# Optimization experiments

Hardware: AMD Instinct MI355X
Metric: run time of the kernel (lower is better)

Reference implementation:

```python
import jax, jax.numpy as jnp
import numpy as np

DIM = 1024
CTX_DIM = 1024
HEADS = 8
DIM_HEAD = 64
INNER = HEADS * DIM_HEAD  # 512
EPS = 1e-5


def _layer_norm(x, gamma, beta):
    mu = jnp.mean(x, axis=-1, keepdims=True)
    var = jnp.mean(jnp.square(x - mu), axis=-1, keepdims=True)
    return (x - mu) * jax.lax.rsqrt(var + EPS) * gamma + beta


def setup_inputs() -> dict:
    key = jax.random.key(0)
    ks = jax.random.split(key, 8)
    b, n, m = 4, 2048, 2048
    x = jax.random.normal(ks[0], (b, n, DIM), dtype=jnp.float32)
    context = jax.random.normal(ks[1], (b, m, CTX_DIM), dtype=jnp.float32)
    Wq = jax.random.normal(ks[2], (DIM, INNER), dtype=jnp.float32) / np.sqrt(DIM)
    Wkv = jax.random.normal(ks[3], (CTX_DIM, 2 * INNER), dtype=jnp.float32) / np.sqrt(CTX_DIM)
    Wout = jax.random.normal(ks[4], (INNER, DIM), dtype=jnp.float32) / np.sqrt(INNER)
    bout = jnp.zeros((DIM,), dtype=jnp.float32)
    g1 = jnp.ones((DIM,), dtype=jnp.float32)
    b1 = jnp.zeros((DIM,), dtype=jnp.float32)
    g2 = jnp.ones((CTX_DIM,), dtype=jnp.float32)
    b2 = jnp.zeros((CTX_DIM,), dtype=jnp.float32)
    return {"x": x, "context": context, "g1": g1, "b1": b1, "g2": g2, "b2": b2,
            "Wq": Wq, "Wkv": Wkv, "Wout": Wout, "bout": bout}


def reference(x, context, g1, b1, g2, b2, Wq, Wkv, Wout, bout):
    b, n, _ = x.shape
    m = context.shape[1]
    scale = DIM_HEAD ** -0.5
    xn = _layer_norm(x, g1, b1)
    cn = _layer_norm(context, g2, b2)
    q = xn @ Wq                      # [b, n, inner]
    kv = cn @ Wkv                    # [b, m, 2*inner]
    k, v = jnp.split(kv, 2, axis=-1)
    # split heads: [b, h, seq, d]
    q = q.reshape(b, n, HEADS, DIM_HEAD).transpose(0, 2, 1, 3)
    k = k.reshape(b, m, HEADS, DIM_HEAD).transpose(0, 2, 1, 3)
    v = v.reshape(b, m, HEADS, DIM_HEAD).transpose(0, 2, 1, 3)
    sim = jnp.einsum('bhid,bhjd->bhij', q, k) * scale
    attn = jax.nn.softmax(sim, axis=-1)
    out = jnp.einsum('bhij,bhjd->bhid', attn, v)
    out = out.transpose(0, 2, 1, 3).reshape(b, n, INNER)
    return out @ Wout + bout
```

## Files before the change

### kernel.cpp

```cpp
#include <hip/hip_runtime.h>
#include <hip/hip_bf16.h>

typedef __bf16 bf16_t;
typedef bf16_t bf16x4 __attribute__((ext_vector_type(4)));
typedef bf16_t bf16x8 __attribute__((ext_vector_type(8)));
typedef float floatx4 __attribute__((ext_vector_type(4)));

typedef __attribute__((address_space(1))) const unsigned char* gptr_t;
typedef __attribute__((address_space(3))) unsigned char* lptr_t;

#define BATCH 4
#define SEQ_N 2048
#define SEQ_M 2048
#define DIM 1024
#define INNER 512
#define HEADS 8
#define DHEAD 64
#define QSCALE 0.18033688011112042f

__device__ __forceinline__ void wtrans_tile(const float* W, bf16_t* Wt,
                                            int K, int N, int n0, int k0, float scale) {
    __shared__ bf16_t T[64][72];
    const int tid = threadIdx.x;
#pragma unroll
    for (int p = 0; p < 2; p++) {
        int r = (tid >> 3) + p * 32;
        int c = (tid & 7) * 8;
        const float* src = W + (size_t)(k0 + r) * N + n0 + c;
        float4 v0 = *(const float4*)src;
        float4 v1 = *(const float4*)(src + 4);
        T[r][c + 0] = (bf16_t)(v0.x * scale); T[r][c + 1] = (bf16_t)(v0.y * scale);
        T[r][c + 2] = (bf16_t)(v0.z * scale); T[r][c + 3] = (bf16_t)(v0.w * scale);
        T[r][c + 4] = (bf16_t)(v1.x * scale); T[r][c + 5] = (bf16_t)(v1.y * scale);
        T[r][c + 6] = (bf16_t)(v1.z * scale); T[r][c + 7] = (bf16_t)(v1.w * scale);
    }
    __syncthreads();
#pragma unroll
    for (int p = 0; p < 2; p++) {
        int rn = (tid >> 3) + p * 32;
        int ck = (tid & 7) * 8;
        bf16x8 v;
#pragma unroll
        for (int i = 0; i < 8; i++) v[i] = T[ck + i][rn];
        *(bf16x8*)(Wt + (size_t)(n0 + rn) * K + k0 + ck) = v;
    }
}

__device__ __forceinline__ void ln_row(const float* in, const float* g,
                                       const float* bt, bf16_t* out, int row) {
    const int tid = threadIdx.x;
    float4 xv = ((const float4*)(in + (size_t)row * 1024))[tid];
    float s = xv.x + xv.y + xv.z + xv.w;
    float ss = xv.x * xv.x + xv.y * xv.y + xv.z * xv.z + xv.w * xv.w;
#pragma unroll
    for (int off = 32; off > 0; off >>= 1) {
        s  += __shfl_down(s, off);
        ss += __shfl_down(ss, off);
    }
    __shared__ float red[8];
    const int wave = tid >> 6, lane = tid & 63;
    if (lane == 0) { red[wave] = s; red[4 + wave] = ss; }
    __syncthreads();
    if (tid == 0) {
        float a = red[0] + red[1] + red[2] + red[3];
        float b = red[4] + red[5] + red[6] + red[7];
        red[0] = a * (1.f / 1024.f);
        red[4] = b * (1.f / 1024.f);
    }
    __syncthreads();
    const float mu = red[0];
    const float var = red[4] - mu * mu;
    const float rs = rsqrtf(var + 1e-5f);

    float4 gv = ((const float4*)g)[tid];
    float4 bv = ((const float4*)bt)[tid];
    bf16x4 o;
    o[0] = (bf16_t)((xv.x - mu) * rs * gv.x + bv.x);
    o[1] = (bf16_t)((xv.y - mu) * rs * gv.y + bv.y);
    o[2] = (bf16_t)((xv.z - mu) * rs * gv.z + bv.z);
    o[3] = (bf16_t)((xv.w - mu) * rs * gv.w + bv.w);
    *(bf16x4*)(out + (size_t)row * 1024 + tid * 4) = o;
}

__global__ __launch_bounds__(256) void prep_kernel(const float* __restrict__ x,
                                                   const float* __restrict__ ctx,
                                                   const float* __restrict__ g1,
                                                   const float* __restrict__ b1,
                                                   const float* __restrict__ g2,
                                                   const float* __restrict__ b2,
                                                   const float* __restrict__ Wq,
                                                   const float* __restrict__ Wkv,
                                                   const float* __restrict__ Wout,
                                                   bf16_t* __restrict__ xn,
                                                   bf16_t* __restrict__ cn,
                                                   bf16_t* __restrict__ Wqt,
                                                   bf16_t* __restrict__ Wkvt,
                                                   bf16_t* __restrict__ Woutt) {
    int id = blockIdx.x;
    if (id < 128) {
        wtrans_tile(Wq, Wqt, 1024, 512, (id & 7) * 64, (id >> 3) * 64, QSCALE);
    } else if (id < 384) {
        int t = id - 128;
        wtrans_tile(Wkv, Wkvt, 1024, 1024, (t & 15) * 64, (t >> 4) * 64, 1.0f);
    } else if (id < 512) {
        int t = id - 384;
        wtrans_tile(Wout, Woutt, 512, 1024, (t & 15) * 64, (t >> 4) * 64, 1.0f);
    } else {
        int rid = id - 512;
        if (rid < BATCH * SEQ_N) ln_row(x, g1, b1, xn, rid);
        else                     ln_row(ctx, g2, b2, cn, rid - BATCH * SEQ_N);
    }
}

template <int MODE, typename OutT>
__device__ __forceinline__ void gemm_body(const bf16_t* __restrict__ A,
                                          const bf16_t* __restrict__ Bt,
                                          OutT* __restrict__ C,
                                          const float* __restrict__ bias,
                                          int ldC, int K, int row0, int col0) {
    __shared__ bf16_t As[128 * 64];
    __shared__ bf16_t Bs[128 * 64];
    const int tid = threadIdx.x;
    const int wave = tid >> 6, lane = tid & 63;
    const int wr = (wave >> 1) * 64, wc = (wave & 1) * 64;
    const int quad = lane >> 4, l16 = lane & 15;

    floatx4 acc[4][4] = {};

    for (int k0 = 0; k0 < K; k0 += 64) {
#pragma unroll
        for (int p = 0; p < 4; p++) {
            int cA = p * 256 + wave * 64 + lane;
            int rA = cA >> 3, kc = (cA & 7) * 8;
            __builtin_amdgcn_global_load_lds(
                (gptr_t)(A + (size_t)(row0 + rA) * K + k0 + kc),
                (lptr_t)(As + (size_t)(p * 256 + wave * 64) * 8), 16, 0, 0);
            __builtin_amdgcn_global_load_lds(
                (gptr_t)(Bt + (size_t)(col0 + rA) * K + k0 + kc),
                (lptr_t)(Bs + (size_t)(p * 256 + wave * 64) * 8), 16, 0, 0);
        }
        __syncthreads();
#pragma unroll
        for (int kt = 0; kt < 2; kt++) {
            bf16x8 aF[4], bF[4];
#pragma unroll
            for (int i = 0; i < 4; i++)
                aF[i] = *(bf16x8*)&As[(wr + i * 16 + l16) * 64 + kt * 32 + quad * 8];
#pragma unroll
            for (int j = 0; j < 4; j++)
                bF[j] = *(bf16x8*)&Bs[(wc + j * 16 + l16) * 64 + kt * 32 + quad * 8];
#pragma unroll
            for (int i = 0; i < 4; i++)
#pragma unroll
                for (int j = 0; j < 4; j++) {
                    if (MODE == 0)
                        acc[i][j] = __builtin_amdgcn_mfma_f32_16x16x32_bf16(
                            aF[i], bF[j], acc[i][j], 0, 0, 0);
                    else
                        acc[i][j] = __builtin_amdgcn_mfma_f32_16x16x32_bf16(
                            bF[j], aF[i], acc[i][j], 0, 0, 0);
                }
        }
        __syncthreads();
    }

    if (MODE == 0) {
#pragma unroll
        for (int i = 0; i < 4; i++)
#pragma unroll
            for (int j = 0; j < 4; j++) {
                int col = col0 + wc + j * 16 + l16;
                float bv = bias ? bias[col] : 0.f;
#pragma unroll
                for (int r = 0; r < 4; r++) {
                    int row = row0 + wr + i * 16 + quad * 4 + r;
                    C[(size_t)row * ldC + col] = (OutT)(acc[i][j][r] + bv);
                }
            }
    } else {
#pragma unroll
        for (int i = 0; i < 4; i++) {
            int grow = row0 + wr + i * 16 + l16;
            int bat = grow >> 11, m = grow & 2047;
#pragma unroll
            for (int j = 0; j < 4; j++)
#pragma unroll
                for (int r = 0; r < 4; r++) {
                    int d = col0 + wc + j * 16 + quad * 4 + r - 512;
                    C[((size_t)bat * 512 + d) * 2048 + m] = (OutT)acc[i][j][r];
                }
        }
    }
}

__global__ __launch_bounds__(256) void gemm_qkv_kernel(const bf16_t* __restrict__ xn,
                                                       const bf16_t* __restrict__ cn,
                                                       const bf16_t* __restrict__ Wqt,
                                                       const bf16_t* __restrict__ Wkvt,
                                                       bf16_t* __restrict__ qb,
                                                       bf16_t* __restrict__ kvb,
                                                       bf16_t* __restrict__ Vtg) {
    const int bx = blockIdx.x;
    const int row0 = blockIdx.y * 128;
    if (bx < 4)
        gemm_body<0, bf16_t>(xn, Wqt, qb, nullptr, 512, DIM, row0, bx * 128);
    else if (bx < 8)
        gemm_body<0, bf16_t>(cn, Wkvt, kvb, nullptr, 512, DIM, row0, (bx - 4) * 128);
    else
        gemm_body<1, bf16_t>(cn, Wkvt, Vtg, nullptr, 0, DIM, row0, (bx - 4) * 128);
}

__global__ __launch_bounds__(256) void gemm_out_kernel(const bf16_t* __restrict__ ao,
                                                       const bf16_t* __restrict__ Woutt,
                                                       float* __restrict__ out,
                                                       const float* __restrict__ bias) {
    gemm_body<0, float>(ao, Woutt, out, bias, DIM, INNER, blockIdx.y * 128, blockIdx.x * 128);
}

#define PSTR 72
__global__ __launch_bounds__(256) void attn_kernel(const bf16_t* __restrict__ q,
                                                   const bf16_t* __restrict__ kv,
                                                   const bf16_t* __restrict__ Vtg,
                                                   bf16_t* __restrict__ o) {
    __shared__ bf16_t Qs[64 * 72];
    __shared__ bf16_t Ks[64 * 72];
    __shared__ bf16_t Vs[80 * 72];

    const int b = blockIdx.z, h = blockIdx.y;
    const int n0 = blockIdx.x * 64;
    const int tid = threadIdx.x;
    const int wave = tid >> 6, lane = tid & 63;
    const int quad = lane >> 4, l16 = lane & 15;

    const int sr = (tid >> 3);
    const int sc = (tid & 7) * 8;

#pragma unroll
    for (int p = 0; p < 2; p++) {
        int r = sr + p * 32;
        *(bf16x8*)&Qs[r * 72 + sc] =
            *(const bf16x8*)(q + (size_t)(b * SEQ_N + n0 + r) * INNER + h * DHEAD + sc);
    }
#pragma unroll
    for (int i = 0; i < 4; i++) {
        int idx = i * 256 + tid;
        int r = 64 + (idx >> 6), c = idx & 63;
        Vs[r * 72 + c] = (r == 64) ? (bf16_t)1.0f : (bf16_t)0.0f;
    }

    bf16x8 kreg[2], vreg[2];
#pragma unroll
    for (int p = 0; p < 2; p++) {
        int r = sr + p * 32;
        kreg[p] = *(const bf16x8*)(kv + (size_t)(b * SEQ_M + r) * 512 + h * DHEAD + sc);
        vreg[p] = *(const bf16x8*)(Vtg + (size_t)((b * HEADS + h) * DHEAD + r) * SEQ_M + sc);
    }
    __syncthreads();

    bf16x8 aQ[2];
#pragma unroll
    for (int kt = 0; kt < 2; kt++)
        aQ[kt] = *(bf16x8*)&Qs[(wave * 16 + l16) * 72 + kt * 32 + quad * 8];

    bf16_t* Pw = Qs + wave * (16 * PSTR);

    floatx4 oacc[5] = {};

    for (int it = 0; it < SEQ_M / 64; ++it) {
        __syncthreads();
#pragma unroll
        for (int p = 0; p < 2; p++) {
            int r = sr + p * 32;
            *(bf16x8*)&Ks[r * 72 + sc] = kreg[p];
            *(bf16x8*)&Vs[r * 72 + sc] = vreg[p];
        }
        __syncthreads();

        if (it + 1 < SEQ_M / 64) {
            int m0 = (it + 1) * 64;
#pragma unroll
            for (int p = 0; p < 2; p++) {
                int r = sr + p * 32;
                kreg[p] = *(const bf16x8*)(kv + (size_t)(b * SEQ_M + m0 + r) * 512 + h * DHEAD + sc);
                vreg[p] = *(const bf16x8*)(Vtg + (size_t)((b * HEADS + h) * DHEAD + r) * SEQ_M + m0 + sc);
            }
        }

        floatx4 s[4] = {};
#pragma unroll
        for (int kt = 0; kt < 2; kt++)
#pragma unroll
            for (int jt = 0; jt < 4; jt++) {
                bf16x8 aK = *(bf16x8*)&Ks[(jt * 16 + l16) * 72 + kt * 32 + quad * 8];
                s[jt] = __builtin_amdgcn_mfma_f32_16x16x32_bf16(aK, aQ[kt], s[jt], 0, 0, 0);
            }

#pragma unroll
        for (int jt = 0; jt < 4; jt++) {
            bf16x4 pk;
#pragma unroll
            for (int r = 0; r < 4; r++) pk[r] = (bf16_t)exp2f(s[jt][r]);
            *(bf16x4*)&Pw[l16 * PSTR + jt * 16 + quad * 4] = pk;
        }

#pragma unroll
        for (int kt = 0; kt < 2; kt++) {
            bf16x8 aP = *(bf16x8*)&Pw[l16 * PSTR + kt * 32 + quad * 8];
#pragma unroll
            for (int dt = 0; dt < 5; dt++) {
                bf16x8 bV = *(bf16x8*)&Vs[(dt * 16 + l16) * 72 + kt * 32 + quad * 8];
                oacc[dt] = __builtin_amdgcn_mfma_f32_16x16x32_bf16(aP, bV, oacc[dt], 0, 0, 0);
            }
        }
    }

    float inv[4];
#pragma unroll
    for (int r = 0; r < 4; r++) {
        float l = __shfl(oacc[4][r], (int)(lane & 48));
        inv[r] = 1.0f / l;
    }
#pragma unroll
    for (int dt = 0; dt < 4; dt++)
#pragma unroll
        for (int r = 0; r < 4; r++) {
            int row = n0 + wave * 16 + quad * 4 + r;
            int col = h * DHEAD + dt * 16 + l16;
            o[(size_t)(b * SEQ_N + row) * INNER + col] =
                (bf16_t)(oacc[dt][r] * inv[r]);
        }
}

extern "C" void kernel_launch(void* const* d_in, const int* in_sizes, int n_in,
                              void* d_out, int out_size, void* d_ws, size_t ws_size,
                              hipStream_t stream) {
    const float* x    = (const float*)d_in[0];
    const float* ctx  = (const float*)d_in[1];
    const float* g1   = (const float*)d_in[2];
    const float* b1   = (const float*)d_in[3];
    const float* g2   = (const float*)d_in[4];
    const float* b2   = (const float*)d_in[5];
    const float* Wq   = (const float*)d_in[6];
    const float* Wkv  = (const float*)d_in[7];
    const float* Wout = (const float*)d_in[8];
    const float* bout = (const float*)d_in[9];
    float* out = (float*)d_out;

    const int rows = BATCH * SEQ_N;
    bf16_t* xn    = (bf16_t*)d_ws;
    bf16_t* cn    = xn + (size_t)rows * DIM;
    bf16_t* qb    = cn + (size_t)rows * DIM;
    bf16_t* kvb   = qb + (size_t)rows * INNER;
    bf16_t* Vtg   = kvb + (size_t)rows * INNER;
    bf16_t* Wqt   = Vtg + (size_t)rows * INNER;
    bf16_t* Wkvt  = Wqt + (size_t)INNER * DIM;
    bf16_t* Woutt = Wkvt + (size_t)(2 * INNER) * DIM;
    bf16_t* o_attn = xn;

    prep_kernel<<<512 + 2 * rows, 256, 0, stream>>>(
        x, ctx, g1, b1, g2, b2, Wq, Wkv, Wout, xn, cn, Wqt, Wkvt, Woutt);
    gemm_qkv_kernel<<<dim3(12, rows / 128), 256, 0, stream>>>(
        xn, cn, Wqt, Wkvt, qb, kvb, Vtg);
    attn_kernel<<<dim3(SEQ_N / 64, HEADS, BATCH), 256, 0, stream>>>(qb, kvb, Vtg, o_attn);
    gemm_out_kernel<<<dim3(DIM / 128, rows / 128), 256, 0, stream>>>(o_attn, Woutt, out, bout);
}
```

Measured before the change: 263.5 us.

## Rework layernorm, V-transpose epilogue, out-GEMM tiling and attention denominator

LayerNorm now has one wave handle a whole row, four rows per block. This drops the block-level shared-memory reduction and both barriers, and cuts the prep grid size. The transposed V store in the QKV GEMM is staged through LDS so it writes 4-wide vector stores instead of scattered scalar bf16 stores. The output GEMM gets a 64-column tile template, which doubles its block count. In attention, the all-ones row used to compute the softmax denominator moves from LDS into a register operand, and the K/V prefetch becomes unconditional. On the last iteration that prefetch reads just past the K/V and V-transposed buffers, into adjacent workspace.

```diff
diff --git a/kernel.cpp b/kernel.cpp
--- a/kernel.cpp
+++ b/kernel.cpp
@@ -46,40 +46,40 @@
     }
 }
 
-__device__ __forceinline__ void ln_row(const float* in, const float* g,
-                                       const float* bt, bf16_t* out, int row) {
-    const int tid = threadIdx.x;
-    float4 xv = ((const float4*)(in + (size_t)row * 1024))[tid];
-    float s = xv.x + xv.y + xv.z + xv.w;
-    float ss = xv.x * xv.x + xv.y * xv.y + xv.z * xv.z + xv.w * xv.w;
+__device__ __forceinline__ void ln_row_wave(const float* in, const float* g,
+                                            const float* bt, bf16_t* out, int row) {
+    const int lane = threadIdx.x & 63;
+    const float4* src = (const float4*)(in + (size_t)row * 1024);
+    float4 xv[4];
+    float s = 0.f, ss = 0.f;
+#pragma unroll
+    for (int k = 0; k < 4; k++) {
+        xv[k] = src[lane + k * 64];
+        s  += xv[k].x + xv[k].y + xv[k].z + xv[k].w;
+        ss += xv[k].x * xv[k].x + xv[k].y * xv[k].y + xv[k].z * xv[k].z + xv[k].w * xv[k].w;
+    }
 #pragma unroll
     for (int off = 32; off > 0; off >>= 1) {
         s  += __shfl_down(s, off);
         ss += __shfl_down(ss, off);
     }
-    __shared__ float red[8];
-    const int wave = tid >> 6, lane = tid & 63;
-    if (lane == 0) { red[wave] = s; red[4 + wave] = ss; }
-    __syncthreads();
-    if (tid == 0) {
-        float a = red[0] + red[1] + red[2] + red[3];
-        float b = red[4] + red[5] + red[6] + red[7];
-        red[0] = a * (1.f / 1024.f);
-        red[4] = b * (1.f / 1024.f);
-    }
-    __syncthreads();
-    const float mu = red[0];
-    const float var = red[4] - mu * mu;
+    s  = __shfl(s, 0);
+    ss = __shfl(ss, 0);
+    const float mu = s * (1.f / 1024.f);
+    const float var = ss * (1.f / 1024.f) - mu * mu;
     const float rs = rsqrtf(var + 1e-5f);
-
-    float4 gv = ((const float4*)g)[tid];
-    float4 bv = ((const float4*)bt)[tid];
-    bf16x4 o;
-    o[0] = (bf16_t)((xv.x - mu) * rs * gv.x + bv.x);
-    o[1] = (bf16_t)((xv.y - mu) * rs * gv.y + bv.y);
-    o[2] = (bf16_t)((xv.z - mu) * rs * gv.z + bv.z);
-    o[3] = (bf16_t)((xv.w - mu) * rs * gv.w + bv.w);
-    *(bf16x4*)(out + (size_t)row * 1024 + tid * 4) = o;
+    const float4* gp = (const float4*)g;
+    const float4* bp = (const float4*)bt;
+#pragma unroll
+    for (int k = 0; k < 4; k++) {
+        float4 gv = gp[lane + k * 64], bv = bp[lane + k * 64];
+        bf16x4 o;
+        o[0] = (bf16_t)((xv[k].x - mu) * rs * gv.x + bv.x);
+        o[1] = (bf16_t)((xv[k].y - mu) * rs * gv.y + bv.y);
+        o[2] = (bf16_t)((xv[k].z - mu) * rs * gv.z + bv.z);
+        o[3] = (bf16_t)((xv[k].w - mu) * rs * gv.w + bv.w);
+        *(bf16x4*)(out + (size_t)row * 1024 + (lane + k * 64) * 4) = o;
+    }
 }
 
 __global__ __launch_bounds__(256) void prep_kernel(const float* __restrict__ x,
@@ -106,26 +106,28 @@
         int t = id - 384;
         wtrans_tile(Wout, Woutt, 512, 1024, (t & 15) * 64, (t >> 4) * 64, 1.0f);
     } else {
-        int rid = id - 512;
-        if (rid < BATCH * SEQ_N) ln_row(x, g1, b1, xn, rid);
-        else                     ln_row(ctx, g2, b2, cn, rid - BATCH * SEQ_N);
-    }
-}
-
-template <int MODE, typename OutT>
+        int row = (id - 512) * 4 + (threadIdx.x >> 6);
+        if (row < BATCH * SEQ_N) ln_row_wave(x, g1, b1, xn, row);
+        else                     ln_row_wave(ctx, g2, b2, cn, row - BATCH * SEQ_N);
+    }
+}
+
+template <int NT, int MODE, typename OutT>
 __device__ __forceinline__ void gemm_body(const bf16_t* __restrict__ A,
                                           const bf16_t* __restrict__ Bt,
                                           OutT* __restrict__ C,
                                           const float* __restrict__ bias,
                                           int ldC, int K, int row0, int col0) {
     __shared__ bf16_t As[128 * 64];
-    __shared__ bf16_t Bs[128 * 64];
+    __shared__ bf16_t Bs[NT * 64];
     const int tid = threadIdx.x;
     const int wave = tid >> 6, lane = tid & 63;
-    const int wr = (wave >> 1) * 64, wc = (wave & 1) * 64;
+    constexpr int WC = NT / 2;
+    constexpr int NJ = WC / 16;
+    const int wr = (wave >> 1) * 64, wc = (wave & 1) * WC;
     const int quad = lane >> 4, l16 = lane & 15;
 
-    floatx4 acc[4][4] = {};
+    floatx4 acc[4][NJ] = {};
 
     for (int k0 = 0; k0 < K; k0 += 64) {
 #pragma unroll
@@ -135,24 +137,25 @@
             __builtin_amdgcn_global_load_lds(
                 (gptr_t)(A + (size_t)(row0 + rA) * K + k0 + kc),
                 (lptr_t)(As + (size_t)(p * 256 + wave * 64) * 8), 16, 0, 0);
-            __builtin_amdgcn_global_load_lds(
-                (gptr_t)(Bt + (size_t)(col0 + rA) * K + k0 + kc),
-                (lptr_t)(Bs + (size_t)(p * 256 + wave * 64) * 8), 16, 0, 0);
+            if (p < NT / 32)
+                __builtin_amdgcn_global_load_lds(
+                    (gptr_t)(Bt + (size_t)(col0 + rA) * K + k0 + kc),
+                    (lptr_t)(Bs + (size_t)(p * 256 + wave * 64) * 8), 16, 0, 0);
         }
         __syncthreads();
 #pragma unroll
         for (int kt = 0; kt < 2; kt++) {
-            bf16x8 aF[4], bF[4];
+            bf16x8 aF[4], bF[NJ];
 #pragma unroll
             for (int i = 0; i < 4; i++)
                 aF[i] = *(bf16x8*)&As[(wr + i * 16 + l16) * 64 + kt * 32 + quad * 8];
 #pragma unroll
-            for (int j = 0; j < 4; j++)
+            for (int j = 0; j < NJ; j++)
                 bF[j] = *(bf16x8*)&Bs[(wc + j * 16 + l16) * 64 + kt * 32 + quad * 8];
 #pragma unroll
             for (int i = 0; i < 4; i++)
 #pragma unroll
-                for (int j = 0; j < 4; j++) {
+                for (int j = 0; j < NJ; j++) {
                     if (MODE == 0)
                         acc[i][j] = __builtin_amdgcn_mfma_f32_16x16x32_bf16(
                             aF[i], bF[j], acc[i][j], 0, 0, 0);
@@ -168,7 +171,7 @@
 #pragma unroll
         for (int i = 0; i < 4; i++)
 #pragma unroll
-            for (int j = 0; j < 4; j++) {
+            for (int j = 0; j < NJ; j++) {
                 int col = col0 + wc + j * 16 + l16;
                 float bv = bias ? bias[col] : 0.f;
 #pragma unroll
@@ -178,17 +181,23 @@
                 }
             }
     } else {
-#pragma unroll
-        for (int i = 0; i < 4; i++) {
-            int grow = row0 + wr + i * 16 + l16;
-            int bat = grow >> 11, m = grow & 2047;
+        bf16_t* Tw = (wave < 2 ? As : Bs) + (wave & 1) * 4096;
+#pragma unroll
+        for (int i = 0; i < 4; i++)
 #pragma unroll
             for (int j = 0; j < 4; j++)
 #pragma unroll
-                for (int r = 0; r < 4; r++) {
-                    int d = col0 + wc + j * 16 + quad * 4 + r - 512;
-                    C[((size_t)bat * 512 + d) * 2048 + m] = (OutT)acc[i][j][r];
-                }
+                for (int r = 0; r < 4; r++)
+                    Tw[(j * 16 + quad * 4 + r) * 64 + i * 16 + l16] = (bf16_t)acc[i][j][r];
+        __syncthreads();
+        const int grow = row0 + wr;
+        const int bat = grow >> 11, gm = (grow & 2047) + l16 * 4;
+#pragma unroll
+        for (int dd = 0; dd < 16; dd++) {
+            int d = dd * 4 + quad;
+            bf16x4 v = *(bf16x4*)&Tw[d * 64 + l16 * 4];
+            int gd = col0 + wc + d - 512;
+            *(bf16x4*)(C + ((size_t)bat * 512 + gd) * 2048 + gm) = v;
         }
     }
 }
@@ -203,18 +212,19 @@
     const int bx = blockIdx.x;
     const int row0 = blockIdx.y * 128;
     if (bx < 4)
-        gemm_body<0, bf16_t>(xn, Wqt, qb, nullptr, 512, DIM, row0, bx * 128);
+        gemm_body<128, 0, bf16_t>(xn, Wqt, qb, nullptr, 512, DIM, row0, bx * 128);
     else if (bx < 8)
-        gemm_body<0, bf16_t>(cn, Wkvt, kvb, nullptr, 512, DIM, row0, (bx - 4) * 128);
+        gemm_body<128, 0, bf16_t>(cn, Wkvt, kvb, nullptr, 512, DIM, row0, (bx - 4) * 128);
     else
-        gemm_body<1, bf16_t>(cn, Wkvt, Vtg, nullptr, 0, DIM, row0, (bx - 4) * 128);
+        gemm_body<128, 1, bf16_t>(cn, Wkvt, Vtg, nullptr, 0, DIM, row0, (bx - 4) * 128);
 }
 
 __global__ __launch_bounds__(256) void gemm_out_kernel(const bf16_t* __restrict__ ao,
                                                        const bf16_t* __restrict__ Woutt,
                                                        float* __restrict__ out,
                                                        const float* __restrict__ bias) {
-    gemm_body<0, float>(ao, Woutt, out, bias, DIM, INNER, blockIdx.y * 128, blockIdx.x * 128);
+    gemm_body<64, 0, float>(ao, Woutt, out, bias, DIM, INNER,
+                            blockIdx.y * 128, blockIdx.x * 64);
 }
 
 #define PSTR 72
@@ -224,7 +234,7 @@
                                                    bf16_t* __restrict__ o) {
     __shared__ bf16_t Qs[64 * 72];
     __shared__ bf16_t Ks[64 * 72];
-    __shared__ bf16_t Vs[80 * 72];
+    __shared__ bf16_t Vs[64 * 72];
 
     const int b = blockIdx.z, h = blockIdx.y;
     const int n0 = blockIdx.x * 64;
@@ -241,19 +251,21 @@
         *(bf16x8*)&Qs[r * 72 + sc] =
             *(const bf16x8*)(q + (size_t)(b * SEQ_N + n0 + r) * INNER + h * DHEAD + sc);
     }
-#pragma unroll
-    for (int i = 0; i < 4; i++) {
-        int idx = i * 256 + tid;
-        int r = 64 + (idx >> 6), c = idx & 63;
-        Vs[r * 72 + c] = (r == 64) ? (bf16_t)1.0f : (bf16_t)0.0f;
-    }
-
+
+    bf16x8 bOnes;
+    {
+        bf16_t ov = (l16 == 0) ? (bf16_t)1.0f : (bf16_t)0.0f;
+#pragma unroll
+        for (int i = 0; i < 8; i++) bOnes[i] = ov;
+    }
+
+    const bf16_t* kp = kv + (size_t)(b * SEQ_M) * 512 + h * DHEAD + sc;
+    const bf16_t* vp = Vtg + (size_t)((b * HEADS + h) * DHEAD) * SEQ_M + sc;
     bf16x8 kreg[2], vreg[2];
 #pragma unroll
     for (int p = 0; p < 2; p++) {
-        int r = sr + p * 32;
-        kreg[p] = *(const bf16x8*)(kv + (size_t)(b * SEQ_M + r) * 512 + h * DHEAD + sc);
-        vreg[p] = *(const bf16x8*)(Vtg + (size_t)((b * HEADS + h) * DHEAD + r) * SEQ_M + sc);
+        kreg[p] = *(const bf16x8*)(kp + (size_t)(sr + p * 32) * 512);
+        vreg[p] = *(const bf16x8*)(vp + (size_t)(sr + p * 32) * SEQ_M);
     }
     __syncthreads();
 
@@ -276,14 +288,12 @@
         }
         __syncthreads();
 
-        if (it + 1 < SEQ_M / 64) {
-            int m0 = (it + 1) * 64;
-#pragma unroll
-            for (int p = 0; p < 2; p++) {
-                int r = sr + p * 32;
-                kreg[p] = *(const bf16x8*)(kv + (size_t)(b * SEQ_M + m0 + r) * 512 + h * DHEAD + sc);
-                vreg[p] = *(const bf16x8*)(Vtg + (size_t)((b * HEADS + h) * DHEAD + r) * SEQ_M + m0 + sc);
-            }
+        kp += 64 * 512;
+        vp += 64;
+#pragma unroll
+        for (int p = 0; p < 2; p++) {
+            kreg[p] = *(const bf16x8*)(kp + (size_t)(sr + p * 32) * 512);
+            vreg[p] = *(const bf16x8*)(vp + (size_t)(sr + p * 32) * SEQ_M);
         }
 
         floatx4 s[4] = {};
@@ -307,10 +317,11 @@
         for (int kt = 0; kt < 2; kt++) {
             bf16x8 aP = *(bf16x8*)&Pw[l16 * PSTR + kt * 32 + quad * 8];
 #pragma unroll
-            for (int dt = 0; dt < 5; dt++) {
+            for (int dt = 0; dt < 4; dt++) {
                 bf16x8 bV = *(bf16x8*)&Vs[(dt * 16 + l16) * 72 + kt * 32 + quad * 8];
                 oacc[dt] = __builtin_amdgcn_mfma_f32_16x16x32_bf16(aP, bV, oacc[dt], 0, 0, 0);
             }
+            oacc[4] = __builtin_amdgcn_mfma_f32_16x16x32_bf16(aP, bOnes, oacc[4], 0, 0, 0);
         }
     }
 
@@ -357,10 +368,10 @@
     bf16_t* Woutt = Wkvt + (size_t)(2 * INNER) * DIM;
     bf16_t* o_attn = xn;
 
-    prep_kernel<<<512 + 2 * rows, 256, 0, stream>>>(
+    prep_kernel<<<512 + (2 * rows) / 4, 256, 0, stream>>>(
         x, ctx, g1, b1, g2, b2, Wq, Wkv, Wout, xn, cn, Wqt, Wkvt, Woutt);
     gemm_qkv_kernel<<<dim3(12, rows / 128), 256, 0, stream>>>(
         xn, cn, Wqt, Wkvt, qb, kvb, Vtg);
     attn_kernel<<<dim3(SEQ_N / 64, HEADS, BATCH), 256, 0, stream>>>(qb, kvb, Vtg, o_attn);
-    gemm_out_kernel<<<dim3(DIM / 128, rows / 128), 256, 0, stream>>>(o_attn, Woutt, out, bout);
-}
+    gemm_out_kernel<<<dim3(DIM / 64, rows / 128), 256, 0, stream>>>(o_attn, Woutt, out, bout);
+}
```

New measurement: 259.6 us. Within noise of the previous version (-1.5%).
